# Optimization experiments

Measured on AMD Instinct MI355X. Metric: run time of the kernel, lower is better.

## Reference

```python
import jax, jax.numpy as jnp
import numpy as np

B, S, E, H = 2, 2048, 2048, 16
D = E // H  # head_dim = 128
EPS = 1e-5


def setup_inputs() -> dict:
    key = jax.random.key(0)
    ks = jax.random.split(key, 16)
    s_e = 1.0 / np.sqrt(E)
    s_f = 1.0 / np.sqrt(4 * E)
    return {
        "x": jax.random.normal(ks[0], (B, S, E), jnp.float32),
        "ln1_w": jnp.ones((E,), jnp.float32) + 0.01 * jax.random.normal(ks[1], (E,)),
        "ln1_b": 0.01 * jax.random.normal(ks[2], (E,)),
        "wq": s_e * jax.random.normal(ks[3], (E, E), jnp.float32),
        "wk": s_e * jax.random.normal(ks[4], (E, E), jnp.float32),
        "wv": s_e * jax.random.normal(ks[5], (E, E), jnp.float32),
        "wo": s_e * jax.random.normal(ks[6], (E, E), jnp.float32),
        "bo": 0.01 * jax.random.normal(ks[7], (E,)),
        "ln2_w": jnp.ones((E,), jnp.float32) + 0.01 * jax.random.normal(ks[8], (E,)),
        "ln2_b": 0.01 * jax.random.normal(ks[9], (E,)),
        "w1": s_e * jax.random.normal(ks[10], (E, 4 * E), jnp.float32),
        "b1": 0.01 * jax.random.normal(ks[11], (4 * E,)),
        "w2": s_f * jax.random.normal(ks[12], (4 * E, E), jnp.float32),
        "b2": 0.01 * jax.random.normal(ks[13], (E,)),
    }


def _layernorm(x, w, b):
    mu = jnp.mean(x, axis=-1, keepdims=True)
    var = jnp.var(x, axis=-1, keepdims=True)
    return (x - mu) * jax.lax.rsqrt(var + EPS) * w + b


def _attention(x, wq, wk, wv, wo, bo):
    # x: [B,S,E] -> q,k,v: [B,H,S,D]
    def split(t):
        return t.reshape(B, S, H, D).transpose(0, 2, 1, 3)
    q = split(x @ wq)
    k = split(x @ wk)
    v = split(x @ wv)
    scores = jnp.einsum("bhqd,bhkd->bhqk", q, k)  # [B,H,S,S]
    causal = jnp.triu(jnp.ones((S, S), bool), k=1)
    scores = jnp.where(causal, -jnp.inf, scores)
    # NOTE: faithful to source -- scaling applied after masking, inside softmax arg
    attn = jax.nn.softmax(scores / np.sqrt(D), axis=-1)
    ctx = jnp.einsum("bhqk,bhkd->bhqd", attn, v)
    ctx = ctx.transpose(0, 2, 1, 3).reshape(B, S, E)
    return ctx @ wo + bo


def reference(x, ln1_w, ln1_b, wq, wk, wv, wo, bo, ln2_w, ln2_b, w1, b1, w2, b2):
    shortcut = x
    x1 = _layernorm(x, ln1_w, ln1_b)
    attn_out = _attention(x1, wq, wk, wv, wo, bo)
    a = attn_out + shortcut
    # NOTE: faithful to source quirk -- second shortcut is post-LN1 x1, not a
    y = _layernorm(a, ln2_w, ln2_b)
    y = jax.nn.gelu(y @ w1 + b1, approximate=False) @ w2 + b2
    return x1 + y
```

## Files before the change

kernel.cpp:

```cpp
#include <hip/hip_runtime.h>
#include <math.h>

typedef unsigned short u16;
typedef unsigned int u32;
typedef __attribute__((ext_vector_type(8))) short short8;
typedef __attribute__((ext_vector_type(4))) float f32x4;
typedef __attribute__((ext_vector_type(16))) float f32x16;
typedef __attribute__((ext_vector_type(4))) u32 u32x4;
typedef __attribute__((ext_vector_type(2))) u32 u32x2;

#define DEVFN static __device__ __forceinline__

DEVFN u16 f2bf(float x) {
  union { float f; u32 u; } v; v.f = x;
  u32 r = v.u + 0x7fffu + ((v.u >> 16) & 1u);
  return (u16)(r >> 16);
}
DEVFN float bf2f(u16 h) {
  union { u32 u; float f; } v; v.u = ((u32)h) << 16;
  return v.f;
}
DEVFN u32 packbf2(float a, float b) {
  return (u32)f2bf(a) | ((u32)f2bf(b) << 16);
}
DEVFN void gl2lds16(const u16* g, u16* l) {
  __builtin_amdgcn_global_load_lds(
      (const __attribute__((address_space(1))) u32*)g,
      (__attribute__((address_space(3))) u32*)l, 16, 0, 0);
}
DEVFN float gelu_exact(float v) {
  float s = v * 0.70710678118654752f;
  float ax = fabsf(s);
  float t = __builtin_amdgcn_rcpf(1.0f + 0.3275911f * ax);
  float poly = t * (0.254829592f +
               t * (-0.284496736f +
               t * (1.421413741f +
               t * (-1.453152027f + t * 1.061405429f))));
  float e = __expf(-s * s);
  float er = 1.0f - poly * e;
  er = (s < 0.f) ? -er : er;
  return 0.5f * v * (1.0f + er);
}

#define VMW4() asm volatile("s_waitcnt vmcnt(4)" ::: "memory")
#define VMW2() asm volatile("s_waitcnt vmcnt(2)" ::: "memory")
#define VMW0() asm volatile("s_waitcnt vmcnt(0)" ::: "memory")
#define CFENCE() asm volatile("" ::: "memory")
#define BARRIER() do { CFENCE(); __builtin_amdgcn_s_barrier(); CFENCE(); } while (0)

__global__ __launch_bounds__(256) void tconvall_k(
    const float* __restrict__ wq, const float* __restrict__ wk,
    const float* __restrict__ wv, const float* __restrict__ wo,
    const float* __restrict__ w1, const float* __restrict__ w2,
    u16* __restrict__ wqt, u16* __restrict__ wkt, u16* __restrict__ wvt,
    u16* __restrict__ wot, u16* __restrict__ w1t, u16* __restrict__ w2t) {
  __shared__ float tile[32][33];
  int b = blockIdx.x;
  const float* in; u16* out; int K, N, tn, tk;
  if (b < 16384) {
    int wsel = b >> 12;
    int loc = b & 4095;
    in = (wsel == 0) ? wq : (wsel == 1) ? wk : (wsel == 2) ? wv : wo;
    out = (wsel == 0) ? wqt : (wsel == 1) ? wkt : (wsel == 2) ? wvt : wot;
    K = 2048; N = 2048; tn = loc & 63; tk = loc >> 6;
  } else if (b < 32768) {
    int loc = b - 16384; in = w1; out = w1t; K = 2048; N = 8192;
    tn = loc & 255; tk = loc >> 8;
  } else {
    int loc = b - 32768; in = w2; out = w2t; K = 8192; N = 2048;
    tn = loc & 63; tk = loc >> 6;
  }
  int n0 = tn << 5, k0 = tk << 5;
  int tx = threadIdx.x & 31, ty = threadIdx.x >> 5;
#pragma unroll
  for (int i = 0; i < 32; i += 8)
    tile[ty + i][tx] = in[(long)(k0 + ty + i) * N + n0 + tx];
  __syncthreads();
#pragma unroll
  for (int i = 0; i < 32; i += 8)
    out[(long)(n0 + ty + i) * K + k0 + tx] = f2bf(tile[tx][ty + i]);
}

__global__ __launch_bounds__(256) void ln1_k(const float* __restrict__ x,
                                             const float* __restrict__ w,
                                             const float* __restrict__ b,
                                             float* __restrict__ y32,
                                             u16* __restrict__ y16) {
  long base = (long)blockIdx.x * 2048;
  int t = threadIdx.x;
  float4 v0 = ((const float4*)(x + base))[2 * t];
  float4 v1 = ((const float4*)(x + base))[2 * t + 1];
  float xv[8];
  *(float4*)xv = v0; *(float4*)(xv + 4) = v1;
  float s = 0.f, ss = 0.f;
#pragma unroll
  for (int i = 0; i < 8; ++i) { s += xv[i]; ss += xv[i] * xv[i]; }
#pragma unroll
  for (int m = 1; m < 64; m <<= 1) { s += __shfl_xor(s, m); ss += __shfl_xor(ss, m); }
  __shared__ float rs[4], rss[4];
  int wave = t >> 6;
  if ((t & 63) == 0) { rs[wave] = s; rss[wave] = ss; }
  __syncthreads();
  s = rs[0] + rs[1] + rs[2] + rs[3];
  ss = rss[0] + rss[1] + rss[2] + rss[3];
  float mean = s * (1.f / 2048.f);
  float var = ss * (1.f / 2048.f) - mean * mean;
  float inv = rsqrtf(var + 1e-5f);
  float wv[8], bv[8];
  *(float4*)wv = ((const float4*)w)[2 * t]; *(float4*)(wv + 4) = ((const float4*)w)[2 * t + 1];
  *(float4*)bv = ((const float4*)b)[2 * t]; *(float4*)(bv + 4) = ((const float4*)b)[2 * t + 1];
  float yv[8];
#pragma unroll
  for (int i = 0; i < 8; ++i) yv[i] = (xv[i] - mean) * inv * wv[i] + bv[i];
  ((float4*)(y32 + base))[2 * t] = *(float4*)yv;
  ((float4*)(y32 + base))[2 * t + 1] = *(float4*)(yv + 4);
  u32x4 ov;
#pragma unroll
  for (int i = 0; i < 4; ++i) ov[i] = packbf2(yv[2 * i], yv[2 * i + 1]);
  ((u32x4*)(y16 + base))[t] = ov;
}

__global__ __launch_bounds__(256) void ln2_k(const u16* __restrict__ a,
                                             const float* __restrict__ w,
                                             const float* __restrict__ b,
                                             u16* __restrict__ y) {
  long base = (long)blockIdx.x * 2048;
  int t = threadIdx.x;
  u32x4 pv = ((const u32x4*)(a + base))[t];
  float xv[8];
#pragma unroll
  for (int i = 0; i < 4; ++i) {
    xv[2 * i] = bf2f((u16)(pv[i] & 0xffffu));
    xv[2 * i + 1] = bf2f((u16)(pv[i] >> 16));
  }
  float s = 0.f, ss = 0.f;
#pragma unroll
  for (int i = 0; i < 8; ++i) { s += xv[i]; ss += xv[i] * xv[i]; }
#pragma unroll
  for (int m = 1; m < 64; m <<= 1) { s += __shfl_xor(s, m); ss += __shfl_xor(ss, m); }
  __shared__ float rs[4], rss[4];
  int wave = t >> 6;
  if ((t & 63) == 0) { rs[wave] = s; rss[wave] = ss; }
  __syncthreads();
  s = rs[0] + rs[1] + rs[2] + rs[3];
  ss = rss[0] + rss[1] + rss[2] + rss[3];
  float mean = s * (1.f / 2048.f);
  float var = ss * (1.f / 2048.f) - mean * mean;
  float inv = rsqrtf(var + 1e-5f);
  float wv[8], bv[8];
  *(float4*)wv = ((const float4*)w)[2 * t]; *(float4*)(wv + 4) = ((const float4*)w)[2 * t + 1];
  *(float4*)bv = ((const float4*)b)[2 * t]; *(float4*)(bv + 4) = ((const float4*)b)[2 * t + 1];
  u32x4 ov;
#pragma unroll
  for (int i = 0; i < 4; ++i) {
    float y0 = (xv[2 * i] - mean) * inv * wv[2 * i] + bv[2 * i];
    float y1 = (xv[2 * i + 1] - mean) * inv * wv[2 * i + 1] + bv[2 * i + 1];
    ov[i] = packbf2(y0, y1);
  }
  ((u32x4*)(y + base))[t] = ov;
}

template <int MODE, int IM>
__global__ __launch_bounds__(512, 2) void gemm8_k(const u16* __restrict__ A,
                                                  const u16* __restrict__ W,
                                                  void* __restrict__ outp,
                                                  const float* __restrict__ bias,
                                                  const float* __restrict__ resid,
                                                  int M, int N, int K) {
  constexpr int BM = IM * 32;
  constexpr int BN = 256;
  __shared__ __align__(16) u16 lds[2][(BM + BN) * 64];
  const int t = threadIdx.x, lane = t & 63, wave = t >> 6;
  const int g = lane >> 4, r16 = lane & 15;
  const int wm = wave >> 2, wn = wave & 3;
  const int nM = M / BM;
  const int nwg = gridDim.x * gridDim.y;
  const int orig = blockIdx.y * gridDim.x + blockIdx.x;
  const int sw = (nwg & 7) ? orig : ((orig & 7) * (nwg >> 3) + (orig >> 3));
  const long m0 = (long)(sw % nM) * BM, n0 = (long)(sw / nM) * BN;
  const int nt = K >> 6;
  const long Kl = K;

  auto stA = [&](int b, int half, int tile) {
#pragma unroll
    for (int q = 0; q < 2; ++q) {
      int rl = (wave * 2 + q) * 8 + (lane >> 3);
      int c = (lane & 7) ^ (rl & 7);
      gl2lds16(A + (m0 + half * 128 + rl) * Kl + ((long)tile << 6) + c * 8,
               &lds[b][half * 8192 + (wave * 2 + q) * 512]);
    }
  };
  auto stB = [&](int b, int half, int tile) {
#pragma unroll
    for (int q = 0; q < 2; ++q) {
      int rl = (wave * 2 + q) * 8 + (lane >> 3);
      int c = (lane & 7) ^ (rl & 7);
      gl2lds16(W + (n0 + half * 128 + rl) * Kl + ((long)tile << 6) + c * 8,
               &lds[b][BM * 64 + half * 8192 + (wave * 2 + q) * 512]);
    }
  };

  f32x4 acc[IM][4] = {};
  short8 af[4][2], bf[2][2];

#define LDAF(IH)                                                              \
  _Pragma("unroll") for (int ii2 = 0; ii2 < 4; ++ii2) {                       \
    int row = (((IH)*4 + ii2) * 2 + wm) * 16 + r16;                           \
    _Pragma("unroll") for (int kk = 0; kk < 2; ++kk)                          \
        af[ii2][kk] = *(const short8*)(&lds[cur][row * 64 +                   \
                                        (((kk << 2) | g) ^ (row & 7)) * 8]);  \
  }
#define LDBF(JH)                                                              \
  _Pragma("unroll") for (int jj2 = 0; jj2 < 2; ++jj2) {                       \
    int row = (((JH)*2 + jj2) * 4 + wn) * 16 + r16;                           \
    _Pragma("unroll") for (int kk = 0; kk < 2; ++kk)                          \
        bf[jj2][kk] = *(const short8*)(&lds[cur][BM * 64 + row * 64 +         \
                                        (((kk << 2) | g) ^ (row & 7)) * 8]);  \
  }
#define MFMA_PH(IH, JH)                                                       \
  __builtin_amdgcn_s_setprio(1);                                              \
  _Pragma("unroll") for (int ii2 = 0; ii2 < 4; ++ii2)                         \
      _Pragma("unroll") for (int jj2 = 0; jj2 < 2; ++jj2)                     \
          _Pragma("unroll") for (int kk = 0; kk < 2; ++kk)                    \
              acc[(IH)*4 + ii2][(JH)*2 + jj2] =                               \
                  __builtin_amdgcn_mfma_f32_16x16x32_bf16(                    \
                      af[ii2][kk], bf[jj2][kk],                               \
                      acc[(IH)*4 + ii2][(JH)*2 + jj2], 0, 0, 0);              \
  __builtin_amdgcn_s_setprio(0);

  if constexpr (IM == 8) {
    stA(0, 0, 0); stB(0, 0, 0); stB(0, 1, 0); stA(0, 1, 0);
    VMW4();
  } else {
    stA(0, 0, 0); stB(0, 0, 0); stB(0, 1, 0);
    VMW2();
  }
  BARRIER();

  for (int tt = 0; tt < nt; ++tt) {
    const int cur = tt & 1, nxt = cur ^ 1;
    const int ts = (tt + 1 < nt) ? tt + 1 : tt;
    if constexpr (IM == 8) {
      LDAF(0); LDBF(0);
      stA(nxt, 0, ts);
      MFMA_PH(0, 0);
      VMW4(); BARRIER();
      LDBF(1);
      stB(nxt, 0, ts);
      MFMA_PH(0, 1);
      VMW4(); BARRIER();
      LDAF(1); LDBF(0);
      stB(nxt, 1, ts);
      MFMA_PH(1, 0);
      BARRIER();
      LDBF(1);
      stA(nxt, 1, ts);
      MFMA_PH(1, 1);
      VMW4(); BARRIER();
    } else {
      LDAF(0); LDBF(0);
      stA(nxt, 0, ts); stB(nxt, 0, ts);
      MFMA_PH(0, 0);
      VMW4(); BARRIER();
      LDBF(1);
      stB(nxt, 1, ts);
      MFMA_PH(0, 1);
      VMW2(); BARRIER();
    }
  }
  VMW0();

  const long Nl = N;
#pragma unroll
  for (int ii = 0; ii < IM; ++ii) {
#pragma unroll
    for (int jj = 0; jj < 4; ++jj) {
#pragma unroll
      for (int r = 0; r < 4; ++r) {
        long mg = m0 + (ii * 2 + wm) * 16 + g * 4 + r;
        long ng = n0 + (jj * 4 + wn) * 16 + r16;
        float v = acc[ii][jj][r];
        if constexpr (MODE == 0) {
          long which = ng >> 11;
          long nloc = ng & 2047;
          long bb = mg >> 11, sq = mg & 2047;
          long hh = nloc >> 7, dd = nloc & 127;
          long idx = (which < 2) ? (((bb * 16 + hh) * 2048 + sq) * 128 + dd)
                                 : (((bb * 16 + hh) * 128 + dd) * 2048 + sq);
          ((u16*)outp)[which * 8388608 + idx] = f2bf(v);
        } else if constexpr (MODE == 2) {
          v += bias[ng] + resid[mg * Nl + ng];
          ((u16*)outp)[mg * Nl + ng] = f2bf(v);
        } else if constexpr (MODE == 3) {
          v = gelu_exact(v + bias[ng]);
          ((u16*)outp)[mg * Nl + ng] = f2bf(v);
        } else {
          v += bias[ng] + resid[mg * Nl + ng];
          ((float*)outp)[mg * Nl + ng] = v;
        }
      }
    }
  }
#undef LDAF
#undef LDBF
#undef MFMA_PH
}

__global__ __launch_bounds__(256, 2) void attn2_k(const u16* __restrict__ Qp,
                                                  const u16* __restrict__ Kp,
                                                  const u16* __restrict__ Vp,
                                                  u16* __restrict__ ctx) {
  __shared__ __align__(16) u16 KsL[2][64 * 128];
  __shared__ __align__(16) u16 VsL[2][128 * 64];
  const int qt = gridDim.x - 1 - blockIdx.x;
  const int bh = blockIdx.y;
  const int t = threadIdx.x, lane = t & 63, wave = t >> 6;
  const int l31 = lane & 31, hi = lane >> 5;
  const int q0 = qt * 128, qw0 = q0 + wave * 32;
  const int qg = qw0 + l31;
  const u16* Qh = Qp + (long)bh * 2048 * 128;
  const u16* Kh = Kp + (long)bh * 2048 * 128;
  const u16* Vh = Vp + (long)bh * 128 * 2048;
  const int nkt = qt * 2 + 2;
  const int ktmax = (qw0 + 31) >> 6;
  const float cs = 0.12753042923810058f;

  short8 qf[8];
#pragma unroll
  for (int ds = 0; ds < 8; ++ds)
    qf[ds] = *(const short8*)(Qh + (long)qg * 128 + ds * 16 + hi * 8);

  f32x16 O0 = {}, O1 = {}, O2 = {}, O3 = {};
  float m = -INFINITY, l = 0.f;

  auto stage = [&](int b, int kt) {
#pragma unroll
    for (int q = 0; q < 4; ++q) {
      int r = wave * 16 + q * 4 + (lane >> 4);
      int c = (lane & 15) ^ (r & 15);
      gl2lds16(Kh + ((long)kt * 64 + r) * 128 + c * 8,
               &KsL[b][(wave * 16 + q * 4) * 128]);
    }
#pragma unroll
    for (int q = 0; q < 4; ++q) {
      int r = wave * 32 + q * 8 + (lane >> 3);
      int c = (lane & 7) ^ (r & 7);
      gl2lds16(Vh + (long)r * 2048 + kt * 64 + c * 8,
               &VsL[b][(wave * 32 + q * 8) * 64]);
    }
  };

  stage(0, 0);
  VMW0(); BARRIER();

  for (int kt = 0; kt < nkt; ++kt) {
    const int cur = kt & 1;
    if (kt + 1 < nkt) stage(cur ^ 1, kt + 1);
    if (kt <= ktmax) {
      f32x16 S0 = {}, S1 = {};
      __builtin_amdgcn_s_setprio(1);
#pragma unroll
      for (int ds = 0; ds < 8; ++ds) {
        int c0 = ((ds * 2 + hi) ^ (l31 & 15)) * 8;
        short8 k0 = *(const short8*)(&KsL[cur][l31 * 128 + c0]);
        int r1 = 32 + l31;
        int c1 = ((ds * 2 + hi) ^ (r1 & 15)) * 8;
        short8 k1 = *(const short8*)(&KsL[cur][r1 * 128 + c1]);
        S0 = __builtin_amdgcn_mfma_f32_32x32x16_bf16(k0, qf[ds], S0, 0, 0, 0);
        S1 = __builtin_amdgcn_mfma_f32_32x32x16_bf16(k1, qf[ds], S1, 0, 0, 0);
      }
      __builtin_amdgcn_s_setprio(0);
      float p[32];
#pragma unroll
      for (int i = 0; i < 16; ++i) { p[i] = S0[i]; p[16 + i] = S1[i]; }
      if (kt * 64 + 63 > qw0) {
#pragma unroll
        for (int ks = 0; ks < 2; ++ks)
#pragma unroll
          for (int r = 0; r < 16; ++r) {
            int kg = kt * 64 + ks * 32 + (r & 3) + 8 * (r >> 2) + 4 * hi;
            if (kg > qg) p[ks * 16 + r] = -INFINITY;
          }
      }
      float tmax = p[0];
#pragma unroll
      for (int i = 1; i < 32; ++i) tmax = fmaxf(tmax, p[i]);
      tmax = fmaxf(tmax, __shfl_xor(tmax, 32));
      float mnew = fmaxf(m, tmax);
      float corr = __builtin_amdgcn_exp2f((m - mnew) * cs);
      float ls = 0.f;
#pragma unroll
      for (int i = 0; i < 32; ++i) {
        p[i] = __builtin_amdgcn_exp2f((p[i] - mnew) * cs);
        ls += p[i];
      }
      ls += __shfl_xor(ls, 32);
      l = l * corr + ls;
      m = mnew;
#pragma unroll
      for (int i = 0; i < 16; ++i) {
        O0[i] *= corr; O1[i] *= corr; O2[i] *= corr; O3[i] *= corr;
      }
      short8 pf[4];
#pragma unroll
      for (int gg = 0; gg < 4; ++gg) {
        u32 u_, v_, w_, z_;
        asm("v_cvt_pk_bf16_f32 %0, %1, %2" : "=v"(u_) : "v"(p[gg * 8 + 0]), "v"(p[gg * 8 + 1]));
        asm("v_cvt_pk_bf16_f32 %0, %1, %2" : "=v"(v_) : "v"(p[gg * 8 + 2]), "v"(p[gg * 8 + 3]));
        asm("v_cvt_pk_bf16_f32 %0, %1, %2" : "=v"(w_) : "v"(p[gg * 8 + 4]), "v"(p[gg * 8 + 5]));
        asm("v_cvt_pk_bf16_f32 %0, %1, %2" : "=v"(z_) : "v"(p[gg * 8 + 6]), "v"(p[gg * 8 + 7]));
        asm("v_permlane32_swap_b32 %0, %1" : "+v"(u_), "+v"(w_));
        asm("v_permlane32_swap_b32 %0, %1" : "+v"(v_), "+v"(z_));
        union { u32 w4[4]; short8 s; } cv;
        cv.w4[0] = u_; cv.w4[1] = v_; cv.w4[2] = w_; cv.w4[3] = z_;
        pf[gg] = cv.s;
      }
      __builtin_amdgcn_s_setprio(1);
#define PVROW(ds, OO)                                                          \
  {                                                                            \
    int row = (ds)*32 + l31;                                                   \
    _Pragma("unroll") for (int gg = 0; gg < 4; ++gg) {                         \
      short8 vf = *(const short8*)(&VsL[cur][row * 64 +                        \
                                             (((gg * 2 + hi) ^ (row & 7)) * 8)]); \
      OO = __builtin_amdgcn_mfma_f32_32x32x16_bf16(vf, pf[gg], OO, 0, 0, 0);   \
    }                                                                          \
  }
      PVROW(0, O0); PVROW(1, O1); PVROW(2, O2); PVROW(3, O3);
#undef PVROW
      __builtin_amdgcn_s_setprio(0);
    }
    VMW0(); BARRIER();
  }

  const float inv = 1.f / l;
  u16* cp = ctx + ((long)(bh >> 4) * 2048 + qg) * 2048 + (bh & 15) * 128;
#define WROUT(OO, dsb)                                                         \
  _Pragma("unroll") for (int rg = 0; rg < 4; ++rg) {                           \
    int d = (dsb)*32 + 8 * rg + 4 * hi;                                        \
    u32x2 wv;                                                                  \
    wv[0] = packbf2(OO[4 * rg] * inv, OO[4 * rg + 1] * inv);                   \
    wv[1] = packbf2(OO[4 * rg + 2] * inv, OO[4 * rg + 3] * inv);               \
    *(u32x2*)(cp + d) = wv;                                                    \
  }
  WROUT(O0, 0); WROUT(O1, 1); WROUT(O2, 2); WROUT(O3, 3);
#undef WROUT
}

extern "C" void kernel_launch(void* const* d_in, const int* in_sizes, int n_in,
                              void* d_out, int out_size, void* d_ws, size_t ws_size,
                              hipStream_t stream) {
  const float* x = (const float*)d_in[0];
  const float* ln1w = (const float*)d_in[1];
  const float* ln1b = (const float*)d_in[2];
  const float* wq = (const float*)d_in[3];
  const float* wk = (const float*)d_in[4];
  const float* wv = (const float*)d_in[5];
  const float* wo = (const float*)d_in[6];
  const float* bo = (const float*)d_in[7];
  const float* ln2w = (const float*)d_in[8];
  const float* ln2b = (const float*)d_in[9];
  const float* w1 = (const float*)d_in[10];
  const float* b1 = (const float*)d_in[11];
  const float* w2 = (const float*)d_in[12];
  const float* b2 = (const float*)d_in[13];
  float* out = (float*)d_out;
  char* ws = (char*)d_ws;

  float* x1f = (float*)(ws + 0);
  u16* x1b = (u16*)(ws + 33554432);
  u16* wqt = (u16*)(ws + 50331648);
  u16* wkt = (u16*)(ws + 58720256);
  u16* wvt = (u16*)(ws + 67108864);
  u16* wot = (u16*)(ws + 75497472);
  u16* w1t = (u16*)(ws + 83886080);
  u16* w2t = (u16*)(ws + 117440512);
  u16* qb = (u16*)(ws + 150994944);
  u16* kb = (u16*)(ws + 167772160);
  u16* vb = (u16*)(ws + 184549376);
  u16* ctxb = (u16*)(ws + 201326592);
  u16* ab = (u16*)(ws + 218103808);
  u16* y0b = (u16*)(ws + 234881024);
  u16* hb = qb;

  tconvall_k<<<49152, 256, 0, stream>>>(wq, wk, wv, wo, w1, w2,
                                        wqt, wkt, wvt, wot, w1t, w2t);
  ln1_k<<<4096, 256, 0, stream>>>(x, ln1w, ln1b, x1f, x1b);
  gemm8_k<0, 8><<<dim3(16, 24), 512, 0, stream>>>(x1b, wqt, qb, nullptr, nullptr, 4096, 6144, 2048);
  attn2_k<<<dim3(16, 32), 256, 0, stream>>>(qb, kb, vb, ctxb);
  gemm8_k<2, 4><<<dim3(32, 8), 512, 0, stream>>>(ctxb, wot, ab, bo, x, 4096, 2048, 2048);
  ln2_k<<<4096, 256, 0, stream>>>(ab, ln2w, ln2b, y0b);
  gemm8_k<3, 8><<<dim3(16, 32), 512, 0, stream>>>(y0b, w1t, hb, b1, nullptr, 4096, 8192, 2048);
  gemm8_k<4, 4><<<dim3(32, 8), 512, 0, stream>>>(hb, w2t, out, b2, x1f, 4096, 2048, 8192);
}
```

Baseline: 661.0 us.

## Split-K the FFN down-projection with larger tiles and fuse LN1 into weight conversion

The final GEMM now uses 256-row tiles and splits K into two halves. Each half writes fp32 partials to a scratch buffer that reuses dead weight workspace, and a new reduction kernel adds the partials, bias and residual. LN1 is folded into the weight transpose/convert kernel as extra blocks to remove a launch. This trades better tile reuse for extra global traffic from writing and re-reading the partials.

Result: faster. 633.0 us, median of 2 (-4.2%).

```diff
diff --git a/kernel.cpp b/kernel.cpp
--- a/kernel.cpp
+++ b/kernel.cpp
@@ -48,14 +48,54 @@
 #define CFENCE() asm volatile("" ::: "memory")
 #define BARRIER() do { CFENCE(); __builtin_amdgcn_s_barrier(); CFENCE(); } while (0)
 
-__global__ __launch_bounds__(256) void tconvall_k(
+__global__ __launch_bounds__(256) void tconvln_k(
     const float* __restrict__ wq, const float* __restrict__ wk,
     const float* __restrict__ wv, const float* __restrict__ wo,
     const float* __restrict__ w1, const float* __restrict__ w2,
     u16* __restrict__ wqt, u16* __restrict__ wkt, u16* __restrict__ wvt,
-    u16* __restrict__ wot, u16* __restrict__ w1t, u16* __restrict__ w2t) {
+    u16* __restrict__ wot, u16* __restrict__ w1t, u16* __restrict__ w2t,
+    const float* __restrict__ x, const float* __restrict__ ln1w,
+    const float* __restrict__ ln1b, float* __restrict__ y32,
+    u16* __restrict__ y16) {
+  int b = blockIdx.x;
+  int t = threadIdx.x;
+  if (b >= 49152) {
+    long base = (long)(b - 49152) * 2048;
+    float4 v0 = ((const float4*)(x + base))[2 * t];
+    float4 v1 = ((const float4*)(x + base))[2 * t + 1];
+    float xv[8];
+    *(float4*)xv = v0; *(float4*)(xv + 4) = v1;
+    float s = 0.f, ss = 0.f;
+#pragma unroll
+    for (int i = 0; i < 8; ++i) { s += xv[i]; ss += xv[i] * xv[i]; }
+#pragma unroll
+    for (int m = 1; m < 64; m <<= 1) { s += __shfl_xor(s, m); ss += __shfl_xor(ss, m); }
+    __shared__ float rs[4], rss[4];
+    int wave = t >> 6;
+    if ((t & 63) == 0) { rs[wave] = s; rss[wave] = ss; }
+    __syncthreads();
+    s = rs[0] + rs[1] + rs[2] + rs[3];
+    ss = rss[0] + rss[1] + rss[2] + rss[3];
+    float mean = s * (1.f / 2048.f);
+    float var = ss * (1.f / 2048.f) - mean * mean;
+    float inv = rsqrtf(var + 1e-5f);
+    float wv8[8], bv[8];
+    *(float4*)wv8 = ((const float4*)ln1w)[2 * t];
+    *(float4*)(wv8 + 4) = ((const float4*)ln1w)[2 * t + 1];
+    *(float4*)bv = ((const float4*)ln1b)[2 * t];
+    *(float4*)(bv + 4) = ((const float4*)ln1b)[2 * t + 1];
+    float yv[8];
+#pragma unroll
+    for (int i = 0; i < 8; ++i) yv[i] = (xv[i] - mean) * inv * wv8[i] + bv[i];
+    ((float4*)(y32 + base))[2 * t] = *(float4*)yv;
+    ((float4*)(y32 + base))[2 * t + 1] = *(float4*)(yv + 4);
+    u32x4 ov;
+#pragma unroll
+    for (int i = 0; i < 4; ++i) ov[i] = packbf2(yv[2 * i], yv[2 * i + 1]);
+    ((u32x4*)(y16 + base))[t] = ov;
+    return;
+  }
   __shared__ float tile[32][33];
-  int b = blockIdx.x;
   const float* in; u16* out; int K, N, tn, tk;
   if (b < 16384) {
     int wsel = b >> 12;
@@ -71,7 +111,7 @@
     tn = loc & 63; tk = loc >> 6;
   }
   int n0 = tn << 5, k0 = tk << 5;
-  int tx = threadIdx.x & 31, ty = threadIdx.x >> 5;
+  int tx = t & 31, ty = t >> 5;
 #pragma unroll
   for (int i = 0; i < 32; i += 8)
     tile[ty + i][tx] = in[(long)(k0 + ty + i) * N + n0 + tx];
@@ -79,45 +119,6 @@
 #pragma unroll
   for (int i = 0; i < 32; i += 8)
     out[(long)(n0 + ty + i) * K + k0 + tx] = f2bf(tile[tx][ty + i]);
-}
-
-__global__ __launch_bounds__(256) void ln1_k(const float* __restrict__ x,
-                                             const float* __restrict__ w,
-                                             const float* __restrict__ b,
-                                             float* __restrict__ y32,
-                                             u16* __restrict__ y16) {
-  long base = (long)blockIdx.x * 2048;
-  int t = threadIdx.x;
-  float4 v0 = ((const float4*)(x + base))[2 * t];
-  float4 v1 = ((const float4*)(x + base))[2 * t + 1];
-  float xv[8];
-  *(float4*)xv = v0; *(float4*)(xv + 4) = v1;
-  float s = 0.f, ss = 0.f;
-#pragma unroll
-  for (int i = 0; i < 8; ++i) { s += xv[i]; ss += xv[i] * xv[i]; }
-#pragma unroll
-  for (int m = 1; m < 64; m <<= 1) { s += __shfl_xor(s, m); ss += __shfl_xor(ss, m); }
-  __shared__ float rs[4], rss[4];
-  int wave = t >> 6;
-  if ((t & 63) == 0) { rs[wave] = s; rss[wave] = ss; }
-  __syncthreads();
-  s = rs[0] + rs[1] + rs[2] + rs[3];
-  ss = rss[0] + rss[1] + rss[2] + rss[3];
-  float mean = s * (1.f / 2048.f);
-  float var = ss * (1.f / 2048.f) - mean * mean;
-  float inv = rsqrtf(var + 1e-5f);
-  float wv[8], bv[8];
-  *(float4*)wv = ((const float4*)w)[2 * t]; *(float4*)(wv + 4) = ((const float4*)w)[2 * t + 1];
-  *(float4*)bv = ((const float4*)b)[2 * t]; *(float4*)(bv + 4) = ((const float4*)b)[2 * t + 1];
-  float yv[8];
-#pragma unroll
-  for (int i = 0; i < 8; ++i) yv[i] = (xv[i] - mean) * inv * wv[i] + bv[i];
-  ((float4*)(y32 + base))[2 * t] = *(float4*)yv;
-  ((float4*)(y32 + base))[2 * t + 1] = *(float4*)(yv + 4);
-  u32x4 ov;
-#pragma unroll
-  for (int i = 0; i < 4; ++i) ov[i] = packbf2(yv[2 * i], yv[2 * i + 1]);
-  ((u32x4*)(y16 + base))[t] = ov;
 }
 
 __global__ __launch_bounds__(256) void ln2_k(const u16* __restrict__ a,
@@ -177,16 +178,27 @@
   const int nwg = gridDim.x * gridDim.y;
   const int orig = blockIdx.y * gridDim.x + blockIdx.x;
   const int sw = (nwg & 7) ? orig : ((orig & 7) * (nwg >> 3) + (orig >> 3));
-  const long m0 = (long)(sw % nM) * BM, n0 = (long)(sw / nM) * BN;
+  const long m0 = (long)(sw % nM) * BM;
+  long n0, k0;
+  int ks = 0;
+  if constexpr (MODE == 5) {
+    int rest = sw / nM;
+    n0 = (long)(rest & 7) * BN;
+    ks = rest >> 3;
+    k0 = (long)ks * 4096;
+  } else {
+    n0 = (long)(sw / nM) * BN;
+    k0 = 0;
+  }
   const int nt = K >> 6;
-  const long Kl = K;
+  const long Kl = (MODE == 5) ? 8192 : K;
 
   auto stA = [&](int b, int half, int tile) {
 #pragma unroll
     for (int q = 0; q < 2; ++q) {
       int rl = (wave * 2 + q) * 8 + (lane >> 3);
       int c = (lane & 7) ^ (rl & 7);
-      gl2lds16(A + (m0 + half * 128 + rl) * Kl + ((long)tile << 6) + c * 8,
+      gl2lds16(A + (m0 + half * 128 + rl) * Kl + k0 + ((long)tile << 6) + c * 8,
                &lds[b][half * 8192 + (wave * 2 + q) * 512]);
     }
   };
@@ -195,7 +207,7 @@
     for (int q = 0; q < 2; ++q) {
       int rl = (wave * 2 + q) * 8 + (lane >> 3);
       int c = (lane & 7) ^ (rl & 7);
-      gl2lds16(W + (n0 + half * 128 + rl) * Kl + ((long)tile << 6) + c * 8,
+      gl2lds16(W + (n0 + half * 128 + rl) * Kl + k0 + ((long)tile << 6) + c * 8,
                &lds[b][BM * 64 + half * 8192 + (wave * 2 + q) * 512]);
     }
   };
@@ -294,6 +306,8 @@
         } else if constexpr (MODE == 3) {
           v = gelu_exact(v + bias[ng]);
           ((u16*)outp)[mg * Nl + ng] = f2bf(v);
+        } else if constexpr (MODE == 5) {
+          ((float*)outp)[(long)ks * 8388608 + mg * 2048 + ng] = v;
         } else {
           v += bias[ng] + resid[mg * Nl + ng];
           ((float*)outp)[mg * Nl + ng] = v;
@@ -304,6 +318,25 @@
 #undef LDAF
 #undef LDBF
 #undef MFMA_PH
+}
+
+__global__ __launch_bounds__(256) void red_k(const float* __restrict__ p,
+                                             const float* __restrict__ bias,
+                                             const float* __restrict__ resid,
+                                             float* __restrict__ out) {
+  long i = (long)blockIdx.x * 256 + threadIdx.x;
+  for (long idx = i; idx < 2097152; idx += 2048 * 256) {
+    float4 a = ((const float4*)p)[idx];
+    float4 b = ((const float4*)(p + 8388608))[idx];
+    float4 r = ((const float4*)resid)[idx];
+    float4 bs = ((const float4*)bias)[idx & 511];
+    float4 o;
+    o.x = a.x + b.x + r.x + bs.x;
+    o.y = a.y + b.y + r.y + bs.y;
+    o.z = a.z + b.z + r.z + bs.z;
+    o.w = a.w + b.w + r.w + bs.w;
+    ((float4*)out)[idx] = o;
+  }
 }
 
 __global__ __launch_bounds__(256, 2) void attn2_k(const u16* __restrict__ Qp,
@@ -481,14 +514,16 @@
   u16* ab = (u16*)(ws + 218103808);
   u16* y0b = (u16*)(ws + 234881024);
   u16* hb = qb;
-
-  tconvall_k<<<49152, 256, 0, stream>>>(wq, wk, wv, wo, w1, w2,
-                                        wqt, wkt, wvt, wot, w1t, w2t);
-  ln1_k<<<4096, 256, 0, stream>>>(x, ln1w, ln1b, x1f, x1b);
+  float* pbuf = (float*)(ws + 50331648);
+
+  tconvln_k<<<53248, 256, 0, stream>>>(wq, wk, wv, wo, w1, w2,
+                                       wqt, wkt, wvt, wot, w1t, w2t,
+                                       x, ln1w, ln1b, x1f, x1b);
   gemm8_k<0, 8><<<dim3(16, 24), 512, 0, stream>>>(x1b, wqt, qb, nullptr, nullptr, 4096, 6144, 2048);
   attn2_k<<<dim3(16, 32), 256, 0, stream>>>(qb, kb, vb, ctxb);
   gemm8_k<2, 4><<<dim3(32, 8), 512, 0, stream>>>(ctxb, wot, ab, bo, x, 4096, 2048, 2048);
   ln2_k<<<4096, 256, 0, stream>>>(ab, ln2w, ln2b, y0b);
   gemm8_k<3, 8><<<dim3(16, 32), 512, 0, stream>>>(y0b, w1t, hb, b1, nullptr, 4096, 8192, 2048);
-  gemm8_k<4, 4><<<dim3(32, 8), 512, 0, stream>>>(hb, w2t, out, b2, x1f, 4096, 2048, 8192);
-}
+  gemm8_k<5, 8><<<dim3(16, 16), 512, 0, stream>>>(hb, w2t, pbuf, nullptr, nullptr, 4096, 2048, 4096);
+  red_k<<<2048, 256, 0, stream>>>(pbuf, b2, x1f, out);
+}
```
